# Kernel tuning notes

Hardware: AMD Instinct MI355X
Metric: run time of the kernel (lower is better)

Reference implementation:

```python
import jax, jax.numpy as jnp
import numpy as np

N, D, V = 4096, 512, 50000
K = 10  # accuracy_slack_size


def setup_inputs() -> dict:
    key = jax.random.key(0)
    k1, k2, k3, k4 = jax.random.split(key, 4)
    logits = jax.random.normal(k1, (N, D), dtype=jnp.float32)
    target = jax.random.randint(k2, (N,), 0, V, dtype=jnp.int64)
    mask = jax.random.randint(k3, (N,), 0, 2, dtype=jnp.int32)
    word_vectors = jax.random.normal(k4, (V, D), dtype=jnp.float32)
    return {"logits": logits, "target": target, "mask": mask, "word_vectors": word_vectors}


def reference(logits, target, mask, word_vectors):
    # Brute-force euclidean kNN: squared distances suffice for neighbor ranking.
    # d2[n, v] = ||x_n||^2 - 2 x_n . w_v + ||w_v||^2   -> [N, V]
    x2 = jnp.sum(logits * logits, axis=-1, keepdims=True)          # [N, 1]
    w2 = jnp.sum(word_vectors * word_vectors, axis=-1)             # [V]
    d2 = x2 - 2.0 * (logits @ word_vectors.T) + w2[None, :]        # [N, V]
    # top-K smallest distances -> indices of K nearest words
    _, words = jax.lax.top_k(-d2, K)                               # [N, K]
    # membership check: is the target word among the K neighbors
    hit = jnp.any(words == target[:, None], axis=-1)               # [N] bool
    m = mask.astype(jnp.float32)
    acc = jnp.sum(m * hit.astype(jnp.float32)) / jnp.sum(m)
    return jnp.reshape(acc, (1,))
```

## Files before the change

### kernel.cpp

```cpp
#include <hip/hip_runtime.h>
#include <stdint.h>

#define N_ROWS 4096
#define DIM    512
#define VOCAB  50000
#define VPAD   50048
#define TOPK   10
#define MARGIN 8.0f
#define ECHUNKS 196

typedef int   i32x4 __attribute__((ext_vector_type(4)));
typedef float f32x4 __attribute__((ext_vector_type(4)));

#define GLOBAL_AS __attribute__((address_space(1)))
#define LDS_AS    __attribute__((address_space(3)))

__device__ __forceinline__ void quant_row(const float* __restrict__ src,
                                          signed char* __restrict__ dst,
                                          int lane, float* rowmax_out,
                                          float* w2_out) {
    const float4* s4 = (const float4*)(src + lane * 8);
    float4 a = s4[0], b = s4[1];
    float mx = fmaxf(fmaxf(fmaxf(fabsf(a.x), fabsf(a.y)), fmaxf(fabsf(a.z), fabsf(a.w))),
                     fmaxf(fmaxf(fabsf(b.x), fabsf(b.y)), fmaxf(fabsf(b.z), fabsf(b.w))));
    float w2 = a.x*a.x + a.y*a.y + a.z*a.z + a.w*a.w
             + b.x*b.x + b.y*b.y + b.z*b.z + b.w*b.w;
    #pragma unroll
    for (int off = 1; off < 64; off <<= 1) {
        mx  = fmaxf(mx, __shfl_xor(mx, off, 64));
        w2 += __shfl_xor(w2, off, 64);
    }
    float inv = 127.0f / fmaxf(mx, 1e-30f);
    int q0 = (int)rintf(a.x * inv), q1 = (int)rintf(a.y * inv);
    int q2 = (int)rintf(a.z * inv), q3 = (int)rintf(a.w * inv);
    int q4 = (int)rintf(b.x * inv), q5 = (int)rintf(b.y * inv);
    int q6 = (int)rintf(b.z * inv), q7 = (int)rintf(b.w * inv);
    uint2 pk;
    pk.x = (q0 & 0xff) | ((q1 & 0xff) << 8) | ((q2 & 0xff) << 16) | ((unsigned)(q3 & 0xff) << 24);
    pk.y = (q4 & 0xff) | ((q5 & 0xff) << 8) | ((q6 & 0xff) << 16) | ((unsigned)(q7 & 0xff) << 24);
    *(uint2*)(dst + lane * 8) = pk;
    *rowmax_out = mx;
    *w2_out = w2;
}

__global__ __launch_bounds__(256) void quantize_x(const float* __restrict__ X,
                                                  signed char* __restrict__ Xq,
                                                  float* __restrict__ sx) {
    int wave = threadIdx.x >> 6, lane = threadIdx.x & 63;
    int row = blockIdx.x * 4 + wave;
    float mx, w2;
    quant_row(X + (size_t)row * DIM, Xq + (size_t)row * DIM, lane, &mx, &w2);
    if (lane == 0) sx[row] = fmaxf(mx, 1e-30f) / 127.0f;
}

__global__ __launch_bounds__(256) void quantize_w(const float* __restrict__ W,
                                                  signed char* __restrict__ Wq,
                                                  float* __restrict__ sw,
                                                  float* __restrict__ w2) {
    int wave = threadIdx.x >> 6, lane = threadIdx.x & 63;
    int row = blockIdx.x * 4 + wave;
    if (row < VOCAB) {
        float mx, s2;
        quant_row(W + (size_t)row * DIM, Wq + (size_t)row * DIM, lane, &mx, &s2);
        if (lane == 0) { sw[row] = fmaxf(mx, 1e-30f) / 127.0f; w2[row] = s2; }
    } else {
        *(uint2*)(Wq + (size_t)row * DIM + lane * 8) = make_uint2(0, 0);
        if (lane == 0) { sw[row] = 0.0f; w2[row] = 1e30f; }
    }
}

__global__ __launch_bounds__(64) void st_kernel(const float* __restrict__ X,
                                                const float* __restrict__ W,
                                                const int* __restrict__ target,
                                                float* __restrict__ st) {
    int n = blockIdx.x;
    int t = target[n];
    const float4* x4 = (const float4*)(X + (size_t)n * DIM);
    const float4* w4 = (const float4*)(W + (size_t)t * DIM);
    int lane = threadIdx.x;
    float4 xa = x4[lane], xb = x4[lane + 64];
    float4 wa = w4[lane], wb = w4[lane + 64];
    float sxw = xa.x*wa.x + xa.y*wa.y + xa.z*wa.z + xa.w*wa.w
              + xb.x*wb.x + xb.y*wb.y + xb.z*wb.z + xb.w*wb.w;
    float sww = wa.x*wa.x + wa.y*wa.y + wa.z*wa.z + wa.w*wa.w
              + wb.x*wb.x + wb.y*wb.y + wb.z*wb.z + wb.w*wb.w;
    #pragma unroll
    for (int off = 32; off > 0; off >>= 1) {
        sxw += __shfl_down(sxw, off, 64);
        sww += __shfl_down(sww, off, 64);
    }
    if (lane == 0) st[n] = sww - 2.0f * sxw;
}

__global__ __launch_bounds__(256) void count_mfma_i8(
        const signed char* __restrict__ Xq, const signed char* __restrict__ Wq,
        const float* __restrict__ sx, const float* __restrict__ sw,
        const float* __restrict__ w2, const float* __restrict__ st,
        const int* __restrict__ target,
        int* __restrict__ cnt_def, int* __restrict__ cnt_unc) {

    __shared__ signed char Als[128 * 64];
    __shared__ signed char Bls[128 * 64];
    __shared__ float w2_s[128];
    __shared__ float sw_s[128];
    __shared__ float st_s[128];
    __shared__ float sx_s[128];
    __shared__ int   t_s[128];
    __shared__ int   pk_s[128];

    const int tid  = threadIdx.x;
    const int wave = tid >> 6, lane = tid & 63;
    const int row0 = blockIdx.x * 128;
    const int col0 = blockIdx.y * 128;

    if (tid < 128) { w2_s[tid] = w2[col0 + tid]; sw_s[tid] = sw[col0 + tid]; pk_s[tid] = 0; }
    else           { st_s[tid - 128] = st[row0 + tid - 128];
                     sx_s[tid - 128] = sx[row0 + tid - 128];
                     t_s[tid - 128]  = target[row0 + tid - 128]; }

    const signed char* ga = Xq + (size_t)(row0 + wave*32 + (lane >> 2)) * DIM + (lane & 3) * 16;
    const signed char* gb = Wq + (size_t)(col0 + wave*32 + (lane >> 2)) * DIM + (lane & 3) * 16;
    signed char* la0 = &Als[(wave*32     ) * 64];
    signed char* la1 = &Als[(wave*32 + 16) * 64];
    signed char* lb0 = &Bls[(wave*32     ) * 64];
    signed char* lb1 = &Bls[(wave*32 + 16) * 64];

    const int q = lane >> 4, c = lane & 15;
    const int wm = wave >> 1, wn = wave & 1;
    const signed char* ap = &Als[(wm*64 + c) * 64 + q * 16];
    const signed char* bp = &Bls[(wn*64 + c) * 64 + q * 16];

    i32x4 acc[4][4];
    #pragma unroll
    for (int i = 0; i < 4; i++)
        #pragma unroll
        for (int j = 0; j < 4; j++) acc[i][j] = (i32x4){0, 0, 0, 0};

    for (int k0 = 0; k0 < DIM; k0 += 64) {
        __builtin_amdgcn_global_load_lds((const GLOBAL_AS void*)(ga + k0),           (LDS_AS void*)la0, 16, 0, 0);
        __builtin_amdgcn_global_load_lds((const GLOBAL_AS void*)(ga + 16*DIM + k0),  (LDS_AS void*)la1, 16, 0, 0);
        __builtin_amdgcn_global_load_lds((const GLOBAL_AS void*)(gb + k0),           (LDS_AS void*)lb0, 16, 0, 0);
        __builtin_amdgcn_global_load_lds((const GLOBAL_AS void*)(gb + 16*DIM + k0),  (LDS_AS void*)lb1, 16, 0, 0);
        __syncthreads();
        i32x4 af[4], bfr[4];
        #pragma unroll
        for (int i = 0; i < 4; i++) af[i]  = *(const i32x4*)(ap + i * 16 * 64);
        #pragma unroll
        for (int j = 0; j < 4; j++) bfr[j] = *(const i32x4*)(bp + j * 16 * 64);
        #pragma unroll
        for (int i = 0; i < 4; i++)
            #pragma unroll
            for (int j = 0; j < 4; j++)
                acc[i][j] = __builtin_amdgcn_mfma_i32_16x16x64_i8(af[i], bfr[j], acc[i][j], 0, 0, 0);
        __syncthreads();
    }

    #pragma unroll
    for (int i = 0; i < 4; i++) {
        #pragma unroll
        for (int reg = 0; reg < 4; reg++) {
            int r = wm*64 + i*16 + q*4 + reg;
            float stv = st_s[r];
            float sxr = sx_s[r];
            int   t   = t_s[r];
            int def = 0, unc = 0;
            #pragma unroll
            for (int j = 0; j < 4; j++) {
                int col_l = wn*64 + j*16 + c;
                float dot = sxr * sw_s[col_l] * (float)acc[i][j][reg];
                float s = w2_s[col_l] - 2.0f * dot;
                int v = col0 + col_l;
                if (v != t) {
                    if      (s < stv - MARGIN) def++;
                    else if (s < stv + MARGIN) unc++;
                }
            }
            int pk = (def << 16) | unc;
            pk += __shfl_xor(pk, 1, 64);
            pk += __shfl_xor(pk, 2, 64);
            pk += __shfl_xor(pk, 4, 64);
            pk += __shfl_xor(pk, 8, 64);
            if (c == 0) atomicAdd(&pk_s[r], pk);
        }
    }
    __syncthreads();
    if (tid < 128) {
        int pk = pk_s[tid];
        if (pk) {
            atomicAdd(&cnt_def[row0 + tid], pk >> 16);
            atomicAdd(&cnt_unc[row0 + tid], pk & 0xffff);
        }
    }
}

__global__ __launch_bounds__(256) void resolve_kernel(const int* __restrict__ cnt_def,
                                                      const int* __restrict__ cnt_unc,
                                                      int* __restrict__ hit,
                                                      int* __restrict__ amb_rows,
                                                      int* __restrict__ amb_count) {
    int n = blockIdx.x * 256 + threadIdx.x;
    if (n >= N_ROWS) return;
    int d = cnt_def[n], u = cnt_unc[n];
    int h;
    if (d >= TOPK) h = 0;
    else if (d + u < TOPK) h = 1;
    else { int idx = atomicAdd(amb_count, 1); amb_rows[idx] = n; h = 2; }
    hit[n] = h;
}

__global__ __launch_bounds__(256) void exact_kernel(const float* __restrict__ X,
                                                    const float* __restrict__ W,
                                                    const float* __restrict__ w2,
                                                    const float* __restrict__ st,
                                                    const int* __restrict__ target,
                                                    const int* __restrict__ amb_rows,
                                                    const int* __restrict__ amb_count,
                                                    int* __restrict__ count_exact) {
    __shared__ float xs[DIM];
    __shared__ int scnt[4];
    const int tid = threadIdx.x, wave = tid >> 6, lane = tid & 63;
    const int nw = amb_count[0] * ECHUNKS;
    for (int w = blockIdx.x; w < nw; w += gridDim.x) {
        const int row   = amb_rows[w / ECHUNKS];
        const int chunk = w % ECHUNKS;
        __syncthreads();
        for (int i = tid; i < DIM; i += 256) xs[i] = X[(size_t)row * DIM + i];
        if (tid < 4) scnt[tid] = 0;
        __syncthreads();
        const float4 xa = *(const float4*)&xs[lane * 8];
        const float4 xb = *(const float4*)&xs[lane * 8 + 4];
        const float stv = st[row];
        const int   t   = target[row];
        int cnt = 0;
        const int v0 = chunk * 256 + wave * 64;
        #pragma unroll 2
        for (int i = 0; i < 64; i++) {
            int v = v0 + i;
            if (v < VOCAB) {
                const float4* wr = (const float4*)(W + (size_t)v * DIM + lane * 8);
                float4 wa = wr[0], wb = wr[1];
                float p = xa.x*wa.x + xa.y*wa.y + xa.z*wa.z + xa.w*wa.w
                        + xb.x*wb.x + xb.y*wb.y + xb.z*wb.z + xb.w*wb.w;
                p += __shfl_xor(p, 1, 64);
                p += __shfl_xor(p, 2, 64);
                p += __shfl_xor(p, 4, 64);
                p += __shfl_xor(p, 8, 64);
                p += __shfl_xor(p, 16, 64);
                p += __shfl_xor(p, 32, 64);
                float s = w2[v] - 2.0f * p;
                if (lane == 0 && v != t && (s < stv || (s == stv && v < t))) cnt++;
            }
        }
        if (lane == 0) scnt[wave] = cnt;
        __syncthreads();
        if (tid == 0)
            atomicAdd(&count_exact[row], scnt[0] + scnt[1] + scnt[2] + scnt[3]);
    }
}

__global__ __launch_bounds__(256) void finalize2(const int* __restrict__ hit,
                                                 const int* __restrict__ count_exact,
                                                 const int* __restrict__ mask,
                                                 float* __restrict__ out) {
    int tid = threadIdx.x;
    int hits = 0, msum = 0;
    for (int n = tid; n < N_ROWS; n += 256) {
        int m = mask[n];
        msum += m;
        int h = hit[n];
        int hv = (h == 2) ? (count_exact[n] < TOPK ? 1 : 0) : h;
        if (m) hits += hv;
    }
    #pragma unroll
    for (int off = 32; off > 0; off >>= 1) {
        hits += __shfl_down(hits, off, 64);
        msum += __shfl_down(msum, off, 64);
    }
    __shared__ int sh[8];
    int wid = tid >> 6, lane = tid & 63;
    if (lane == 0) { sh[wid] = hits; sh[4 + wid] = msum; }
    __syncthreads();
    if (tid == 0) {
        int H = sh[0] + sh[1] + sh[2] + sh[3];
        int M = sh[4] + sh[5] + sh[6] + sh[7];
        out[0] = (float)H / (float)M;
    }
}

#define BM 128
#define BN 128
#define BK 16
#define TM 8
#define TN 8

__global__ __launch_bounds__(64) void w2_kernel_fb(const float* __restrict__ W,
                                                   float* __restrict__ w2) {
    int v = blockIdx.x;
    const float4* w4 = (const float4*)(W + (size_t)v * DIM);
    int lane = threadIdx.x;
    float4 a = w4[lane];
    float4 b = w4[lane + 64];
    float s = a.x*a.x + a.y*a.y + a.z*a.z + a.w*a.w
            + b.x*b.x + b.y*b.y + b.z*b.z + b.w*b.w;
    #pragma unroll
    for (int off = 32; off > 0; off >>= 1) s += __shfl_down(s, off, 64);
    if (lane == 0) w2[v] = s;
}

__global__ __launch_bounds__(256) void count_kernel_fb(
        const float* __restrict__ X, const float* __restrict__ W,
        const float* __restrict__ w2, const float* __restrict__ st,
        const int* __restrict__ target, int* __restrict__ count) {
    __shared__ float Xs[BK][BM];
    __shared__ float Ws[BK][BN];
    __shared__ float st_s[BM];
    __shared__ int   t_s[BM];
    __shared__ float w2_s[BN];
    const int tid  = threadIdx.x;
    const int row0 = blockIdx.y * BM;
    const int col0 = blockIdx.x * BN;
    if (tid < 128) { st_s[tid] = st[row0 + tid]; t_s[tid] = target[row0 + tid]; }
    else { int cc = tid - 128; int v = col0 + cc; if (v >= VOCAB) v = VOCAB - 1; w2_s[cc] = w2[v]; }
    float acc[TM][TN] = {};
    const int tx = tid & 15;
    const int ty = tid >> 4;
    for (int k0 = 0; k0 < DIM; k0 += BK) {
        #pragma unroll
        for (int j = 0; j < 2; j++) {
            int idx = tid + 256 * j;
            int r   = idx >> 2;
            int kq  = idx & 3;
            float4 xv = *(const float4*)(X + (size_t)(row0 + r) * DIM + k0 + kq * 4);
            Xs[kq*4+0][r] = xv.x; Xs[kq*4+1][r] = xv.y;
            Xs[kq*4+2][r] = xv.z; Xs[kq*4+3][r] = xv.w;
            int v = col0 + r; if (v >= VOCAB) v = VOCAB - 1;
            float4 wv = *(const float4*)(W + (size_t)v * DIM + k0 + kq * 4);
            Ws[kq*4+0][r] = wv.x; Ws[kq*4+1][r] = wv.y;
            Ws[kq*4+2][r] = wv.z; Ws[kq*4+3][r] = wv.w;
        }
        __syncthreads();
        #pragma unroll
        for (int kk = 0; kk < BK; kk++) {
            float a[TM], b[TN];
            #pragma unroll
            for (int i = 0; i < TM; i++) a[i] = Xs[kk][ty * TM + i];
            #pragma unroll
            for (int j = 0; j < TN; j++) b[j] = Ws[kk][tx * TN + j];
            #pragma unroll
            for (int i = 0; i < TM; i++)
                #pragma unroll
                for (int j = 0; j < TN; j++)
                    acc[i][j] += a[i] * b[j];
        }
        __syncthreads();
    }
    int cnt[TM];
    #pragma unroll
    for (int i = 0; i < TM; i++) {
        cnt[i] = 0;
        float stv = st_s[ty * TM + i];
        int   t   = t_s[ty * TM + i];
        #pragma unroll
        for (int j = 0; j < TN; j++) {
            int v = col0 + tx * TN + j;
            float s = w2_s[tx * TN + j] - 2.0f * acc[i][j];
            if (v < VOCAB && v != t && (s < stv || (s == stv && v < t))) cnt[i]++;
        }
    }
    __syncthreads();
    int* scnt = (int*)Xs;
    #pragma unroll
    for (int i = 0; i < TM; i++) scnt[(ty * TM + i) * 16 + tx] = cnt[i];
    __syncthreads();
    if (tid < BM) {
        int s = 0;
        #pragma unroll
        for (int j = 0; j < 16; j++) s += scnt[tid * 16 + j];
        atomicAdd(&count[row0 + tid], s);
    }
}

__global__ __launch_bounds__(256) void finalize_fb(const int* __restrict__ count,
                                                   const int* __restrict__ mask,
                                                   float* __restrict__ out) {
    int tid = threadIdx.x;
    int hits = 0, msum = 0;
    for (int n = tid; n < N_ROWS; n += 256) {
        int m = mask[n];
        msum += m;
        if (m && count[n] < TOPK) hits++;
    }
    #pragma unroll
    for (int off = 32; off > 0; off >>= 1) {
        hits += __shfl_down(hits, off, 64);
        msum += __shfl_down(msum, off, 64);
    }
    __shared__ int sh[8];
    int wid = tid >> 6, lane = tid & 63;
    if (lane == 0) { sh[wid] = hits; sh[4 + wid] = msum; }
    __syncthreads();
    if (tid == 0) {
        int H = sh[0] + sh[1] + sh[2] + sh[3];
        int M = sh[4] + sh[5] + sh[6] + sh[7];
        out[0] = (float)H / (float)M;
    }
}

extern "C" void kernel_launch(void* const* d_in, const int* in_sizes, int n_in,
                              void* d_out, int out_size, void* d_ws, size_t ws_size,
                              hipStream_t stream) {
    const float* X      = (const float*)d_in[0];
    const int*   target = (const int*)d_in[1];
    const int*   mask   = (const int*)d_in[2];
    const float* W      = (const float*)d_in[3];
    float* out = (float*)d_out;
    char* ws = (char*)d_ws;

    const size_t oXq   = 0;
    const size_t oWq   = oXq  + (size_t)N_ROWS * DIM;
    const size_t osx   = oWq  + (size_t)VPAD  * DIM;
    const size_t osw   = osx  + (size_t)N_ROWS * 4;
    const size_t ow2   = osw  + (size_t)VPAD * 4;
    const size_t ost   = ow2  + (size_t)VPAD * 4;
    const size_t ocd   = ost  + (size_t)N_ROWS * 4;
    const size_t ocu   = ocd  + (size_t)N_ROWS * 4;
    const size_t oce   = ocu  + (size_t)N_ROWS * 4;
    const size_t ohit  = oce  + (size_t)N_ROWS * 4;
    const size_t oamb  = ohit + (size_t)N_ROWS * 4;
    const size_t oambc = oamb + (size_t)N_ROWS * 4;
    const size_t need  = oambc + 16;

    if (ws_size >= need) {
        signed char* Xq = (signed char*)(ws + oXq);
        signed char* Wq = (signed char*)(ws + oWq);
        float* sx = (float*)(ws + osx);
        float* sw = (float*)(ws + osw);
        float* w2 = (float*)(ws + ow2);
        float* st = (float*)(ws + ost);
        int* cnt_def = (int*)(ws + ocd);
        int* cnt_unc = (int*)(ws + ocu);
        int* count_exact = (int*)(ws + oce);
        int* hit = (int*)(ws + ohit);
        int* amb_rows = (int*)(ws + oamb);
        int* amb_count = (int*)(ws + oambc);

        hipMemsetAsync(ws + ocd, 0, oambc + 16 - ocd, stream);
        quantize_x<<<N_ROWS / 4, 256, 0, stream>>>(X, Xq, sx);
        quantize_w<<<VPAD / 4, 256, 0, stream>>>(W, Wq, sw, w2);
        st_kernel<<<N_ROWS, 64, 0, stream>>>(X, W, target, st);
        count_mfma_i8<<<dim3(N_ROWS / 128, VPAD / 128), 256, 0, stream>>>(
            Xq, Wq, sx, sw, w2, st, target, cnt_def, cnt_unc);
        resolve_kernel<<<16, 256, 0, stream>>>(cnt_def, cnt_unc, hit, amb_rows, amb_count);
        exact_kernel<<<2048, 256, 0, stream>>>(X, W, w2, st, target, amb_rows, amb_count, count_exact);
        finalize2<<<1, 256, 0, stream>>>(hit, count_exact, mask, out);
    } else {
        float* w2 = (float*)ws;
        float* st = (float*)(ws + 200704);
        int* countp = (int*)(ws + 200704 + 16384);
        hipMemsetAsync(countp, 0, N_ROWS * sizeof(int), stream);
        w2_kernel_fb<<<VOCAB, 64, 0, stream>>>(W, w2);
        st_kernel<<<N_ROWS, 64, 0, stream>>>(X, W, target, st);
        dim3 grid((VOCAB + BN - 1) / BN, N_ROWS / BM);
        count_kernel_fb<<<grid, 256, 0, stream>>>(X, W, w2, st, target, countp);
        finalize_fb<<<1, 256, 0, stream>>>(countp, mask, out);
    }
}
```

Baseline: 457.9 us.

## Fuse prep kernels, swizzle LDS tiles, and band-filter ambiguous rows with int8 prescreen

```diff
diff --git a/kernel.cpp b/kernel.cpp
--- a/kernel.cpp
+++ b/kernel.cpp
@@ -7,10 +7,8 @@
 #define VPAD   50048
 #define TOPK   10
 #define MARGIN 8.0f
-#define ECHUNKS 196
-
-typedef int   i32x4 __attribute__((ext_vector_type(4)));
-typedef float f32x4 __attribute__((ext_vector_type(4)));
+
+typedef int i32x4 __attribute__((ext_vector_type(4)));
 
 #define GLOBAL_AS __attribute__((address_space(1)))
 #define LDS_AS    __attribute__((address_space(3)))
@@ -43,53 +41,56 @@
     *w2_out = w2;
 }
 
-__global__ __launch_bounds__(256) void quantize_x(const float* __restrict__ X,
-                                                  signed char* __restrict__ Xq,
-                                                  float* __restrict__ sx) {
-    int wave = threadIdx.x >> 6, lane = threadIdx.x & 63;
-    int row = blockIdx.x * 4 + wave;
-    float mx, w2;
-    quant_row(X + (size_t)row * DIM, Xq + (size_t)row * DIM, lane, &mx, &w2);
-    if (lane == 0) sx[row] = fmaxf(mx, 1e-30f) / 127.0f;
-}
-
-__global__ __launch_bounds__(256) void quantize_w(const float* __restrict__ W,
-                                                  signed char* __restrict__ Wq,
-                                                  float* __restrict__ sw,
-                                                  float* __restrict__ w2) {
-    int wave = threadIdx.x >> 6, lane = threadIdx.x & 63;
-    int row = blockIdx.x * 4 + wave;
-    if (row < VOCAB) {
-        float mx, s2;
-        quant_row(W + (size_t)row * DIM, Wq + (size_t)row * DIM, lane, &mx, &s2);
-        if (lane == 0) { sw[row] = fmaxf(mx, 1e-30f) / 127.0f; w2[row] = s2; }
+#define PREP_Z  64
+#define PREP_QX (PREP_Z + N_ROWS / 4)
+#define PREP_QW (PREP_QX + VPAD / 4)
+#define PREP_ST (PREP_QW + N_ROWS / 4)
+
+__global__ __launch_bounds__(256) void prep_kernel(
+        const float* __restrict__ X, const float* __restrict__ W,
+        const int* __restrict__ target,
+        signed char* __restrict__ Xq, signed char* __restrict__ Wq,
+        float* __restrict__ sx, float* __restrict__ sw,
+        float* __restrict__ w2, float* __restrict__ st,
+        int* __restrict__ zbase) {
+    const int b = blockIdx.x;
+    const int wave = threadIdx.x >> 6, lane = threadIdx.x & 63;
+    if (b < PREP_Z) {
+        int i = b * 256 + threadIdx.x;
+        if (i < 3 * N_ROWS + 16) zbase[i] = 0;
+    } else if (b < PREP_QX) {
+        int row = (b - PREP_Z) * 4 + wave;
+        float mx, w2v;
+        quant_row(X + (size_t)row * DIM, Xq + (size_t)row * DIM, lane, &mx, &w2v);
+        if (lane == 0) sx[row] = fmaxf(mx, 1e-30f) / 127.0f;
+    } else if (b < PREP_QW) {
+        int row = (b - PREP_QX) * 4 + wave;
+        if (row < VOCAB) {
+            float mx, s2;
+            quant_row(W + (size_t)row * DIM, Wq + (size_t)row * DIM, lane, &mx, &s2);
+            if (lane == 0) { sw[row] = fmaxf(mx, 1e-30f) / 127.0f; w2[row] = s2; }
+        } else {
+            *(uint2*)(Wq + (size_t)row * DIM + lane * 8) = make_uint2(0, 0);
+            if (lane == 0) { sw[row] = 0.0f; w2[row] = 1e30f; }
+        }
     } else {
-        *(uint2*)(Wq + (size_t)row * DIM + lane * 8) = make_uint2(0, 0);
-        if (lane == 0) { sw[row] = 0.0f; w2[row] = 1e30f; }
-    }
-}
-
-__global__ __launch_bounds__(64) void st_kernel(const float* __restrict__ X,
-                                                const float* __restrict__ W,
-                                                const int* __restrict__ target,
-                                                float* __restrict__ st) {
-    int n = blockIdx.x;
-    int t = target[n];
-    const float4* x4 = (const float4*)(X + (size_t)n * DIM);
-    const float4* w4 = (const float4*)(W + (size_t)t * DIM);
-    int lane = threadIdx.x;
-    float4 xa = x4[lane], xb = x4[lane + 64];
-    float4 wa = w4[lane], wb = w4[lane + 64];
-    float sxw = xa.x*wa.x + xa.y*wa.y + xa.z*wa.z + xa.w*wa.w
-              + xb.x*wb.x + xb.y*wb.y + xb.z*wb.z + xb.w*wb.w;
-    float sww = wa.x*wa.x + wa.y*wa.y + wa.z*wa.z + wa.w*wa.w
-              + wb.x*wb.x + wb.y*wb.y + wb.z*wb.z + wb.w*wb.w;
-    #pragma unroll
-    for (int off = 32; off > 0; off >>= 1) {
-        sxw += __shfl_down(sxw, off, 64);
-        sww += __shfl_down(sww, off, 64);
-    }
-    if (lane == 0) st[n] = sww - 2.0f * sxw;
+        int n = (b - PREP_QW) * 4 + wave;
+        int t = target[n];
+        const float4* x4 = (const float4*)(X + (size_t)n * DIM);
+        const float4* w4 = (const float4*)(W + (size_t)t * DIM);
+        float4 xa = x4[lane], xb = x4[lane + 64];
+        float4 wa = w4[lane], wb = w4[lane + 64];
+        float sxw = xa.x*wa.x + xa.y*wa.y + xa.z*wa.z + xa.w*wa.w
+                  + xb.x*wb.x + xb.y*wb.y + xb.z*wb.z + xb.w*wb.w;
+        float sww = wa.x*wa.x + wa.y*wa.y + wa.z*wa.z + wa.w*wa.w
+                  + wb.x*wb.x + wb.y*wb.y + wb.z*wb.z + wb.w*wb.w;
+        #pragma unroll
+        for (int off = 32; off > 0; off >>= 1) {
+            sxw += __shfl_down(sxw, off, 64);
+            sww += __shfl_down(sww, off, 64);
+        }
+        if (lane == 0) st[n] = sww - 2.0f * sxw;
+    }
 }
 
 __global__ __launch_bounds__(256) void count_mfma_i8(
@@ -118,17 +119,19 @@
                      sx_s[tid - 128] = sx[row0 + tid - 128];
                      t_s[tid - 128]  = target[row0 + tid - 128]; }
 
-    const signed char* ga = Xq + (size_t)(row0 + wave*32 + (lane >> 2)) * DIM + (lane & 3) * 16;
-    const signed char* gb = Wq + (size_t)(col0 + wave*32 + (lane >> 2)) * DIM + (lane & 3) * 16;
+    const int ch = (lane & 3) ^ ((lane >> 3) & 3);
+    const signed char* ga = Xq + (size_t)(row0 + wave*32 + (lane >> 2)) * DIM + ch * 16;
+    const signed char* gb = Wq + (size_t)(col0 + wave*32 + (lane >> 2)) * DIM + ch * 16;
     signed char* la0 = &Als[(wave*32     ) * 64];
     signed char* la1 = &Als[(wave*32 + 16) * 64];
     signed char* lb0 = &Bls[(wave*32     ) * 64];
     signed char* lb1 = &Bls[(wave*32 + 16) * 64];
 
     const int q = lane >> 4, c = lane & 15;
+    const int fs = (c >> 1) & 3;
     const int wm = wave >> 1, wn = wave & 1;
-    const signed char* ap = &Als[(wm*64 + c) * 64 + q * 16];
-    const signed char* bp = &Bls[(wn*64 + c) * 64 + q * 16];
+    const signed char* ap = &Als[(wm*64 + c) * 64 + (q ^ fs) * 16];
+    const signed char* bp = &Bls[(wn*64 + c) * 64 + (q ^ fs) * 16];
 
     i32x4 acc[4][4];
     #pragma unroll
@@ -193,72 +196,84 @@
     }
 }
 
-__global__ __launch_bounds__(256) void resolve_kernel(const int* __restrict__ cnt_def,
-                                                      const int* __restrict__ cnt_unc,
-                                                      int* __restrict__ hit,
-                                                      int* __restrict__ amb_rows,
-                                                      int* __restrict__ amb_count) {
+__global__ __launch_bounds__(256) void resolve3(const int* __restrict__ cnt_def,
+                                                const int* __restrict__ cnt_unc,
+                                                int* __restrict__ amb_rows,
+                                                int* __restrict__ amb_count) {
     int n = blockIdx.x * 256 + threadIdx.x;
     if (n >= N_ROWS) return;
     int d = cnt_def[n], u = cnt_unc[n];
-    int h;
-    if (d >= TOPK) h = 0;
-    else if (d + u < TOPK) h = 1;
-    else { int idx = atomicAdd(amb_count, 1); amb_rows[idx] = n; h = 2; }
-    hit[n] = h;
-}
-
-__global__ __launch_bounds__(256) void exact_kernel(const float* __restrict__ X,
-                                                    const float* __restrict__ W,
-                                                    const float* __restrict__ w2,
-                                                    const float* __restrict__ st,
-                                                    const int* __restrict__ target,
-                                                    const int* __restrict__ amb_rows,
-                                                    const int* __restrict__ amb_count,
-                                                    int* __restrict__ count_exact) {
-    __shared__ float xs[DIM];
-    __shared__ int scnt[4];
-    const int tid = threadIdx.x, wave = tid >> 6, lane = tid & 63;
-    const int nw = amb_count[0] * ECHUNKS;
-    for (int w = blockIdx.x; w < nw; w += gridDim.x) {
-        const int row   = amb_rows[w / ECHUNKS];
-        const int chunk = w % ECHUNKS;
-        __syncthreads();
-        for (int i = tid; i < DIM; i += 256) xs[i] = X[(size_t)row * DIM + i];
-        if (tid < 4) scnt[tid] = 0;
-        __syncthreads();
-        const float4 xa = *(const float4*)&xs[lane * 8];
-        const float4 xb = *(const float4*)&xs[lane * 8 + 4];
-        const float stv = st[row];
-        const int   t   = target[row];
-        int cnt = 0;
-        const int v0 = chunk * 256 + wave * 64;
-        #pragma unroll 2
-        for (int i = 0; i < 64; i++) {
-            int v = v0 + i;
-            if (v < VOCAB) {
-                const float4* wr = (const float4*)(W + (size_t)v * DIM + lane * 8);
-                float4 wa = wr[0], wb = wr[1];
-                float p = xa.x*wa.x + xa.y*wa.y + xa.z*wa.z + xa.w*wa.w
-                        + xb.x*wb.x + xb.y*wb.y + xb.z*wb.z + xb.w*wb.w;
+    if (d < TOPK && d + u >= TOPK) {
+        int idx = atomicAdd(amb_count, 1);
+        amb_rows[idx] = n;
+    }
+}
+
+__device__ __forceinline__ int dot4i8(int a, int b, int acc) {
+#if __has_builtin(__builtin_amdgcn_sdot4)
+    return __builtin_amdgcn_sdot4(a, b, acc, false);
+#else
+    #pragma unroll
+    for (int j = 0; j < 4; j++)
+        acc += (int)(signed char)(a >> (8*j)) * (int)(signed char)(b >> (8*j));
+    return acc;
+#endif
+}
+
+__global__ __launch_bounds__(256) void band_scan(
+        const signed char* __restrict__ Xq, const signed char* __restrict__ Wq,
+        const float* __restrict__ X, const float* __restrict__ W,
+        const float* __restrict__ sx, const float* __restrict__ sw,
+        const float* __restrict__ w2, const float* __restrict__ st,
+        const int* __restrict__ target,
+        const int* __restrict__ amb_rows, const int* __restrict__ amb_count,
+        int* __restrict__ count_exact) {
+    const int lane = threadIdx.x & 63;
+    const int wid  = (blockIdx.x << 2) | (threadIdx.x >> 6);
+    const int nw   = gridDim.x << 2;
+    const int namb = amb_count[0];
+    for (int a = 0; a < namb; a++) {
+        const int row = amb_rows[a];
+        const int t   = target[row];
+        const float sxr = sx[row], stv = st[row];
+        const int2 xa8 = *(const int2*)(Xq + (size_t)row * DIM + lane * 8);
+        for (int v = wid; v < VPAD; v += nw) {
+            int2 wa8 = *(const int2*)(Wq + (size_t)v * DIM + lane * 8);
+            int acc = dot4i8(xa8.x, wa8.x, 0);
+            acc = dot4i8(xa8.y, wa8.y, acc);
+            acc += __shfl_xor(acc, 1, 64);
+            acc += __shfl_xor(acc, 2, 64);
+            acc += __shfl_xor(acc, 4, 64);
+            acc += __shfl_xor(acc, 8, 64);
+            acc += __shfl_xor(acc, 16, 64);
+            acc += __shfl_xor(acc, 32, 64);
+            if (v == t) continue;
+            float dot = sxr * sw[v] * (float)acc;
+            float s = w2[v] - 2.0f * dot;
+            if (!(s < stv - MARGIN) && (s < stv + MARGIN)) {
+                const float4* xr = (const float4*)(X + (size_t)row * DIM + lane * 8);
+                const float4* wr = (const float4*)(W + (size_t)v   * DIM + lane * 8);
+                float4 x0 = xr[0], x1 = xr[1];
+                float4 w0 = wr[0], w1 = wr[1];
+                float p = x0.x*w0.x + x0.y*w0.y + x0.z*w0.z + x0.w*w0.w
+                        + x1.x*w1.x + x1.y*w1.y + x1.z*w1.z + x1.w*w1.w;
                 p += __shfl_xor(p, 1, 64);
                 p += __shfl_xor(p, 2, 64);
                 p += __shfl_xor(p, 4, 64);
                 p += __shfl_xor(p, 8, 64);
                 p += __shfl_xor(p, 16, 64);
                 p += __shfl_xor(p, 32, 64);
-                float s = w2[v] - 2.0f * p;
-                if (lane == 0 && v != t && (s < stv || (s == stv && v < t))) cnt++;
+                if (lane == 0) {
+                    float se = w2[v] - 2.0f * p;
+                    if (se < stv || (se == stv && v < t)) atomicAdd(&count_exact[row], 1);
+                }
             }
         }
-        if (lane == 0) scnt[wave] = cnt;
-        __syncthreads();
-        if (tid == 0)
-            atomicAdd(&count_exact[row], scnt[0] + scnt[1] + scnt[2] + scnt[3]);
-    }
-}
-
-__global__ __launch_bounds__(256) void finalize2(const int* __restrict__ hit,
+    }
+}
+
+__global__ __launch_bounds__(256) void finalize3(const int* __restrict__ cnt_def,
+                                                 const int* __restrict__ cnt_unc,
                                                  const int* __restrict__ count_exact,
                                                  const int* __restrict__ mask,
                                                  float* __restrict__ out) {
@@ -267,8 +282,11 @@
     for (int n = tid; n < N_ROWS; n += 256) {
         int m = mask[n];
         msum += m;
-        int h = hit[n];
-        int hv = (h == 2) ? (count_exact[n] < TOPK ? 1 : 0) : h;
+        int d = cnt_def[n], u = cnt_unc[n];
+        int hv;
+        if (d >= TOPK) hv = 0;
+        else if (d + u < TOPK) hv = 1;
+        else hv = (d + count_exact[n] < TOPK) ? 1 : 0;
         if (m) hits += hv;
     }
     #pragma unroll
@@ -305,6 +323,29 @@
     #pragma unroll
     for (int off = 32; off > 0; off >>= 1) s += __shfl_down(s, off, 64);
     if (lane == 0) w2[v] = s;
+}
+
+__global__ __launch_bounds__(64) void st_kernel_fb(const float* __restrict__ X,
+                                                   const float* __restrict__ W,
+                                                   const int* __restrict__ target,
+                                                   float* __restrict__ st) {
+    int n = blockIdx.x;
+    int t = target[n];
+    const float4* x4 = (const float4*)(X + (size_t)n * DIM);
+    const float4* w4 = (const float4*)(W + (size_t)t * DIM);
+    int lane = threadIdx.x;
+    float4 xa = x4[lane], xb = x4[lane + 64];
+    float4 wa = w4[lane], wb = w4[lane + 64];
+    float sxw = xa.x*wa.x + xa.y*wa.y + xa.z*wa.z + xa.w*wa.w
+              + xb.x*wb.x + xb.y*wb.y + xb.z*wb.z + xb.w*wb.w;
+    float sww = wa.x*wa.x + wa.y*wa.y + wa.z*wa.z + wa.w*wa.w
+              + wb.x*wb.x + wb.y*wb.y + wb.z*wb.z + wb.w*wb.w;
+    #pragma unroll
+    for (int off = 32; off > 0; off >>= 1) {
+        sxw += __shfl_down(sxw, off, 64);
+        sww += __shfl_down(sww, off, 64);
+    }
+    if (lane == 0) st[n] = sww - 2.0f * sxw;
 }
 
 __global__ __launch_bounds__(256) void count_kernel_fb(
@@ -416,19 +457,18 @@
     float* out = (float*)d_out;
     char* ws = (char*)d_ws;
 
-    const size_t oXq   = 0;
-    const size_t oWq   = oXq  + (size_t)N_ROWS * DIM;
-    const size_t osx   = oWq  + (size_t)VPAD  * DIM;
-    const size_t osw   = osx  + (size_t)N_ROWS * 4;
-    const size_t ow2   = osw  + (size_t)VPAD * 4;
-    const size_t ost   = ow2  + (size_t)VPAD * 4;
-    const size_t ocd   = ost  + (size_t)N_ROWS * 4;
-    const size_t ocu   = ocd  + (size_t)N_ROWS * 4;
-    const size_t oce   = ocu  + (size_t)N_ROWS * 4;
-    const size_t ohit  = oce  + (size_t)N_ROWS * 4;
-    const size_t oamb  = ohit + (size_t)N_ROWS * 4;
-    const size_t oambc = oamb + (size_t)N_ROWS * 4;
-    const size_t need  = oambc + 16;
+    const size_t oXq  = 0;
+    const size_t oWq  = oXq + (size_t)N_ROWS * DIM;
+    const size_t osx  = oWq + (size_t)VPAD  * DIM;
+    const size_t osw  = osx + (size_t)N_ROWS * 4;
+    const size_t ow2  = osw + (size_t)VPAD * 4;
+    const size_t ost  = ow2 + (size_t)VPAD * 4;
+    const size_t ocd  = ost + (size_t)N_ROWS * 4;
+    const size_t ocu  = ocd + (size_t)N_ROWS * 4;
+    const size_t oce  = ocu + (size_t)N_ROWS * 4;
+    const size_t octr = oce + (size_t)N_ROWS * 4;
+    const size_t oamb = octr + 64;
+    const size_t need = oamb + (size_t)N_ROWS * 4;
 
     if (ws_size >= need) {
         signed char* Xq = (signed char*)(ws + oXq);
@@ -440,26 +480,23 @@
         int* cnt_def = (int*)(ws + ocd);
         int* cnt_unc = (int*)(ws + ocu);
         int* count_exact = (int*)(ws + oce);
-        int* hit = (int*)(ws + ohit);
+        int* amb_count = (int*)(ws + octr);
         int* amb_rows = (int*)(ws + oamb);
-        int* amb_count = (int*)(ws + oambc);
-
-        hipMemsetAsync(ws + ocd, 0, oambc + 16 - ocd, stream);
-        quantize_x<<<N_ROWS / 4, 256, 0, stream>>>(X, Xq, sx);
-        quantize_w<<<VPAD / 4, 256, 0, stream>>>(W, Wq, sw, w2);
-        st_kernel<<<N_ROWS, 64, 0, stream>>>(X, W, target, st);
+
+        prep_kernel<<<PREP_ST, 256, 0, stream>>>(X, W, target, Xq, Wq, sx, sw, w2, st, cnt_def);
         count_mfma_i8<<<dim3(N_ROWS / 128, VPAD / 128), 256, 0, stream>>>(
             Xq, Wq, sx, sw, w2, st, target, cnt_def, cnt_unc);
-        resolve_kernel<<<16, 256, 0, stream>>>(cnt_def, cnt_unc, hit, amb_rows, amb_count);
-        exact_kernel<<<2048, 256, 0, stream>>>(X, W, w2, st, target, amb_rows, amb_count, count_exact);
-        finalize2<<<1, 256, 0, stream>>>(hit, count_exact, mask, out);
+        resolve3<<<16, 256, 0, stream>>>(cnt_def, cnt_unc, amb_rows, amb_count);
+        band_scan<<<512, 256, 0, stream>>>(Xq, Wq, X, W, sx, sw, w2, st, target,
+                                           amb_rows, amb_count, count_exact);
+        finalize3<<<1, 256, 0, stream>>>(cnt_def, cnt_unc, count_exact, mask, out);
     } else {
         float* w2 = (float*)ws;
         float* st = (float*)(ws + 200704);
         int* countp = (int*)(ws + 200704 + 16384);
         hipMemsetAsync(countp, 0, N_ROWS * sizeof(int), stream);
         w2_kernel_fb<<<VOCAB, 64, 0, stream>>>(W, w2);
-        st_kernel<<<N_ROWS, 64, 0, stream>>>(X, W, target, st);
+        st_kernel_fb<<<N_ROWS, 64, 0, stream>>>(X, W, target, st);
         dim3 grid((VOCAB + BN - 1) / BN, N_ROWS / BM);
         count_kernel_fb<<<grid, 256, 0, stream>>>(X, W, w2, st, target, countp);
         finalize_fb<<<1, 256, 0, stream>>>(countp, mask, out);
```

Result: faster. 416.4 us (-9.1%).
